# Optimization experiments

Measured on AMD Instinct MI355X. Metric: run time of the kernel, lower is better.

Reference implementation:

```python
import jax, jax.numpy as jnp
import numpy as np

H = 1024
NH = 16
HD = H // NH
TEMP = 0.5
LN_EPS = 1e-5


def setup_inputs() -> dict:
    key = jax.random.key(0)
    ks = jax.random.split(key, 11)
    s = 1.0 / np.sqrt(H)
    return {
        "feat": jax.random.normal(ks[0], (4, 2048, H), dtype=jnp.float32),
        "qw": jax.random.uniform(ks[1], (H, H), jnp.float32, -s, s),
        "qb": jax.random.uniform(ks[2], (H,), jnp.float32, -s, s),
        "kw": jax.random.uniform(ks[3], (H, H), jnp.float32, -s, s),
        "kb": jax.random.uniform(ks[4], (H,), jnp.float32, -s, s),
        "vw": jax.random.uniform(ks[5], (H, H), jnp.float32, -s, s),
        "vb": jax.random.uniform(ks[6], (H,), jnp.float32, -s, s),
        "ow": jax.random.uniform(ks[7], (H, H), jnp.float32, -s, s),
        "ob": jax.random.uniform(ks[8], (H,), jnp.float32, -s, s),
        "ln_g": jnp.ones((H,), jnp.float32),
        "ln_b": jnp.zeros((H,), jnp.float32),
    }


def reference(feat, qw, qb, kw, kb, vw, vb, ow, ob, ln_g, ln_b):
    B, S, _ = feat.shape
    # torch Linear: y = x @ W.T + b
    def split_heads(x):  # [B,S,H] -> [B,NH,S,HD]
        return x.reshape(B, S, NH, HD).transpose(0, 2, 1, 3)

    Q = split_heads(feat @ qw.T + qb)
    K = split_heads(feat @ kw.T + kb)
    V = split_heads(feat @ vw.T + vb)

    # temperature-scaled attention (note: divide by 0.5, NOT 1/sqrt(d))
    scores = jnp.einsum("bhqd,bhkd->bhqk", Q, K) / TEMP
    w = jax.nn.softmax(scores, axis=-1)
    attn = jnp.einsum("bhqk,bhkd->bhqd", w, V)  # [B,NH,S,HD]
    attn = attn.transpose(0, 2, 1, 3).reshape(B, S, H)

    out = attn @ ow.T + ob
    out = jax.nn.relu(out)  # dropout is identity in eval mode
    mu = jnp.mean(out, axis=-1, keepdims=True)
    var = jnp.mean(jnp.square(out - mu), axis=-1, keepdims=True)
    out = (out - mu) * jax.lax.rsqrt(var + LN_EPS) * ln_g + ln_b
    return out
```

## Files before the change

kernel.cpp:

```cpp
#include <hip/hip_runtime.h>
#include <math.h>

#define HDIM 1024
#define NHEAD 16
#define HEADD 64
#define SEQLEN 2048
#define BATCH 4
#define MROWS (BATCH * SEQLEN)
#define LN_EPS 1e-5f
#define QSCALE 2.8853900817779268f

typedef float f32x4 __attribute__((ext_vector_type(4)));
typedef short s16x8 __attribute__((ext_vector_type(8)));
typedef short s16x4 __attribute__((ext_vector_type(4)));
typedef __bf16 bf16x4 __attribute__((ext_vector_type(4)));

#define MFMA16(a, b, c) __builtin_amdgcn_mfma_f32_16x16x32_bf16((a), (b), (c), 0, 0, 0)

#if __has_builtin(__builtin_amdgcn_exp2f)
#define EXP2(x) __builtin_amdgcn_exp2f(x)
#else
#define EXP2(x) exp2f(x)
#endif

__device__ __forceinline__ void load_lds16(const __bf16* g, __bf16* l) {
  __builtin_amdgcn_global_load_lds((const __attribute__((address_space(1))) void*)g,
                                   (__attribute__((address_space(3))) void*)l, 16, 0, 0);
}

__global__ __launch_bounds__(256) void split_k(const float* __restrict__ src,
                                               __bf16* __restrict__ h,
                                               __bf16* __restrict__ l, int n4) {
  int i = blockIdx.x * blockDim.x + threadIdx.x;
  if (i >= n4) return;
  float4 v = reinterpret_cast<const float4*>(src)[i];
  bf16x4 hv, lv;
  hv[0] = (__bf16)v.x; hv[1] = (__bf16)v.y; hv[2] = (__bf16)v.z; hv[3] = (__bf16)v.w;
  lv[0] = (__bf16)(v.x - (float)hv[0]);
  lv[1] = (__bf16)(v.y - (float)hv[1]);
  lv[2] = (__bf16)(v.z - (float)hv[2]);
  lv[3] = (__bf16)(v.w - (float)hv[3]);
  reinterpret_cast<bf16x4*>(h)[i] = hv;
  reinterpret_cast<bf16x4*>(l)[i] = lv;
}

__global__ __launch_bounds__(256) void wsplit_k(
    const float* __restrict__ w0, const float* __restrict__ w1,
    const float* __restrict__ w2, const float* __restrict__ w3,
    __bf16* __restrict__ h0, __bf16* __restrict__ l0, __bf16* __restrict__ h1,
    __bf16* __restrict__ l1, __bf16* __restrict__ h2, __bf16* __restrict__ l2,
    __bf16* __restrict__ h3, __bf16* __restrict__ l3) {
  const int which = blockIdx.y;
  const float* src = which == 0 ? w0 : which == 1 ? w1 : which == 2 ? w2 : w3;
  __bf16* h = which == 0 ? h0 : which == 1 ? h1 : which == 2 ? h2 : h3;
  __bf16* l = which == 0 ? l0 : which == 1 ? l1 : which == 2 ? l2 : l3;
  const int i = blockIdx.x * blockDim.x + threadIdx.x;
  float4 v = reinterpret_cast<const float4*>(src)[i];
  bf16x4 hv, lv;
  hv[0] = (__bf16)v.x; hv[1] = (__bf16)v.y; hv[2] = (__bf16)v.z; hv[3] = (__bf16)v.w;
  lv[0] = (__bf16)(v.x - (float)hv[0]);
  lv[1] = (__bf16)(v.y - (float)hv[1]);
  lv[2] = (__bf16)(v.z - (float)hv[2]);
  lv[3] = (__bf16)(v.w - (float)hv[3]);
  reinterpret_cast<bf16x4*>(h)[i] = hv;
  reinterpret_cast<bf16x4*>(l)[i] = lv;
}

template <int EPI, int PASSES>
__global__ __launch_bounds__(256, PASSES == 2 ? 3 : 2) void gemm3p_k(
    const __bf16* __restrict__ AH, const __bf16* __restrict__ AL,
    const __bf16* __restrict__ BH, const __bf16* __restrict__ BL,
    const float* __restrict__ bias, const float scale, __bf16* __restrict__ CH,
    __bf16* __restrict__ CL, float* __restrict__ CF) {
  __shared__ __bf16 smem[(PASSES == 3) ? 32768 : 24576];

  const int tid = threadIdx.x;
  const int lane = tid & 63;
  const int w = tid >> 6;
  const int fr = lane & 15;
  const int g = lane >> 4;
  const int wm = w >> 1, wn = w & 1;
  const int m0 = blockIdx.x << 7;
  const int n0 = blockIdx.y << 7;

#define GSTAGE(buf, kt)                                                       \
  do {                                                                        \
    const int ke_ = (kt) * 32 + (lane & 3) * 8;                               \
    _Pragma("unroll") for (int c_ = 0; c_ < 2; ++c_) {                        \
      const int rr_ = 32 * w + 16 * c_ + (lane >> 2);                         \
      const int lo_ = (32 * w + 16 * c_) * 32;                                \
      load_lds16(AH + (size_t)(m0 + rr_) * HDIM + ke_, &smem[(buf)*4096 + lo_]); \
      load_lds16(AL + (size_t)(m0 + rr_) * HDIM + ke_, &smem[8192 + (buf)*4096 + lo_]); \
      load_lds16(BH + (size_t)(n0 + rr_) * HDIM + ke_, &smem[16384 + (buf)*4096 + lo_]); \
      if (PASSES == 3)                                                        \
        load_lds16(BL + (size_t)(n0 + rr_) * HDIM + ke_, &smem[24576 + (buf)*4096 + lo_]); \
    }                                                                         \
  } while (0)

  f32x4 acc[4][4] = {};

  GSTAGE(0, 0);
  __syncthreads();

  for (int kt = 0; kt < HDIM / 32; ++kt) {
    const int buf = kt & 1;
    if (kt + 1 < HDIM / 32) GSTAGE(buf ^ 1, kt + 1);

    s16x8 aH[4], aL[4], bH[4], bL[4];
#pragma unroll
    for (int mi = 0; mi < 4; ++mi) {
      const int off = (wm * 64 + mi * 16 + fr) * 32 + g * 8;
      aH[mi] = *reinterpret_cast<const s16x8*>(&smem[buf * 4096 + off]);
      aL[mi] = *reinterpret_cast<const s16x8*>(&smem[8192 + buf * 4096 + off]);
    }
#pragma unroll
    for (int ni = 0; ni < 4; ++ni) {
      const int off = (wn * 64 + ni * 16 + fr) * 32 + g * 8;
      bH[ni] = *reinterpret_cast<const s16x8*>(&smem[16384 + buf * 4096 + off]);
      if (PASSES == 3)
        bL[ni] = *reinterpret_cast<const s16x8*>(&smem[24576 + buf * 4096 + off]);
    }
#pragma unroll
    for (int mi = 0; mi < 4; ++mi)
#pragma unroll
      for (int ni = 0; ni < 4; ++ni) {
        acc[mi][ni] = MFMA16(aH[mi], bH[ni], acc[mi][ni]);
        if (PASSES == 3) acc[mi][ni] = MFMA16(aH[mi], bL[ni], acc[mi][ni]);
        acc[mi][ni] = MFMA16(aL[mi], bH[ni], acc[mi][ni]);
      }
    __syncthreads();
  }

  float bv[4];
#pragma unroll
  for (int ni = 0; ni < 4; ++ni) bv[ni] = bias[n0 + wn * 64 + ni * 16 + fr];

  if (EPI == 0) {
#pragma unroll
    for (int mi = 0; mi < 4; ++mi)
#pragma unroll
      for (int ni = 0; ni < 4; ++ni)
#pragma unroll
        for (int r = 0; r < 4; ++r) {
          const float v = (acc[mi][ni][r] + bv[ni]) * scale;
          const int m = m0 + wm * 64 + mi * 16 + 4 * g + r;
          const int n = n0 + wn * 64 + ni * 16 + fr;
          const int b = m >> 11, s = m & 2047, h = n >> 6, d = n & 63;
          const size_t o = ((size_t)(b * NHEAD + h) * SEQLEN + s) * HEADD + d;
          const __bf16 hb = (__bf16)v;
          CH[o] = hb;
          CL[o] = (__bf16)(v - (float)hb);
        }
  } else if (EPI == 2) {
#pragma unroll
    for (int mi = 0; mi < 4; ++mi)
#pragma unroll
      for (int ni = 0; ni < 4; ++ni)
#pragma unroll
        for (int r = 0; r < 4; ++r) {
          const int m = m0 + wm * 64 + mi * 16 + 4 * g + r;
          const int n = n0 + wn * 64 + ni * 16 + fr;
          CF[(size_t)m * HDIM + n] = acc[mi][ni][r] + bv[ni];
        }
  } else {
    __syncthreads();
#pragma unroll
    for (int mi = 0; mi < 4; ++mi)
#pragma unroll
      for (int ni = 0; ni < 4; ++ni)
#pragma unroll
        for (int r = 0; r < 4; ++r) {
          const float v = acc[mi][ni][r] + bv[ni];
          const int nl = wn * 64 + ni * 16 + fr;
          const int ml = wm * 64 + mi * 16 + 4 * g + r;
          smem[nl * 128 + (((ml >> 3) ^ (nl & 7)) << 3) + (ml & 7)] = (__bf16)v;
        }
    __syncthreads();
    const int nl = tid >> 1, mh = tid & 1;
    const int b = m0 >> 11, s0 = m0 & 2047;
    const int gn = n0 + nl, h = gn >> 6, d = gn & 63;
#pragma unroll
    for (int j = 0; j < 8; ++j) {
      const int cm = mh * 8 + j;
      s16x8 vv = *reinterpret_cast<const s16x8*>(&smem[nl * 128 + ((cm ^ (nl & 7)) << 3)]);
      const size_t o = ((size_t)((b * NHEAD + h) * HEADD + d)) * SEQLEN + s0 + cm * 8;
      *reinterpret_cast<s16x8*>(&CH[o]) = vv;
    }
  }
#undef GSTAGE
}

__global__ __launch_bounds__(256, 2) void attn6_k(
    const __bf16* __restrict__ QH, const __bf16* __restrict__ QL,
    const __bf16* __restrict__ KH, const __bf16* __restrict__ KL,
    const __bf16* __restrict__ VT, __bf16* __restrict__ OH,
    __bf16* __restrict__ OL) {
  __shared__ __bf16 smem[32768];

  const int tid = threadIdx.x;
  const int lane = tid & 63;
  const int w = tid >> 6;
  const int fr = lane & 15;
  const int g = lane >> 4;
  const int f7 = fr & 7;

  const int blk = blockIdx.x;
  const int xcd = blk & 7, idx = blk >> 3;
  const int bh = xcd * 8 + (idx >> 4);
  const int qt = idx & 15;
  const int q0 = qt << 7;
  const size_t bhO = (size_t)bh * SEQLEN * HEADD;

  s16x8 qHf[2][2], qLf[2][2];
#pragma unroll
  for (int qb = 0; qb < 2; ++qb) {
    const size_t qoff = bhO + (size_t)(q0 + w * 32 + qb * 16 + fr) * HEADD;
#pragma unroll
    for (int ks = 0; ks < 2; ++ks) {
      qHf[qb][ks] = *reinterpret_cast<const s16x8*>(&QH[qoff + ks * 32 + g * 8]);
      qLf[qb][ks] = *reinterpret_cast<const s16x8*>(&QL[qoff + ks * 32 + g * 8]);
    }
  }

  const __bf16* gsrc[6];
  int gstep[6], ldoff[6];
  {
    const int rsub = lane >> 3;
    const int ch = (lane & 7) ^ rsub;
#pragma unroll
    for (int i_ = 0; i_ < 6; ++i_) {
      const int L_ = w * 6 + i_;
      const int t_ = L_ >> 3, sub_ = L_ & 7;
      ldoff[i_] = t_ * 8192 + sub_ * 512;
      if (t_ < 2) {
        const __bf16* base_ = (t_ == 0) ? KH : KL;
        gsrc[i_] = base_ + bhO + (size_t)(sub_ * 8 + rsub) * HEADD + ch * 8;
        gstep[i_] = 64 * HEADD;
      } else {
        gsrc[i_] = VT + ((size_t)bh * HEADD + sub_ * 8 + rsub) * SEQLEN + ch * 8;
        gstep[i_] = 64;
      }
    }
  }

#define ASTAGE(bufl)                                              \
  do {                                                            \
    _Pragma("unroll") for (int i_ = 0; i_ < 6; ++i_) {            \
      load_lds16(gsrc[i_], &smem[ldoff[i_] + (bufl)*4096]);       \
      gsrc[i_] += gstep[i_];                                      \
    }                                                             \
  } while (0)

  const int rb0 = fr * 64 + ((g ^ f7) << 3);
  const int rb1 = fr * 64 + (((4 + g) ^ f7) << 3);
  const int prbase = 24576 + w * 2048;
  const int pwbase = 24576 + w * 2048 + fr * 64 + (g & 1) * 4;
  int pco[4];
#pragma unroll
  for (int kb = 0; kb < 4; ++kb) pco[kb] = ((2 * kb + (g >> 1)) ^ f7) << 3;

  f32x4 oacc0[4] = {}, oacc1[4] = {};
  float m0r = -1e30f, m1r = -1e30f, l0r = 0.f, l1r = 0.f;

  auto process = [&](const int B) {
    f32x4 sf0[4] = {}, sf1[4] = {};
    __builtin_amdgcn_s_setprio(1);
#pragma unroll
    for (int kb = 0; kb < 4; ++kb) {
      const s16x8 kh0 = *reinterpret_cast<const s16x8*>(&smem[B * 4096 + kb * 1024 + rb0]);
      const s16x8 kl0 = *reinterpret_cast<const s16x8*>(&smem[8192 + B * 4096 + kb * 1024 + rb0]);
      const s16x8 kh1 = *reinterpret_cast<const s16x8*>(&smem[B * 4096 + kb * 1024 + rb1]);
      const s16x8 kl1 = *reinterpret_cast<const s16x8*>(&smem[8192 + B * 4096 + kb * 1024 + rb1]);
      sf0[kb] = MFMA16(kh0, qHf[0][0], sf0[kb]);
      sf0[kb] = MFMA16(kl0, qHf[0][0], sf0[kb]);
      sf0[kb] = MFMA16(kh0, qLf[0][0], sf0[kb]);
      sf0[kb] = MFMA16(kh1, qHf[0][1], sf0[kb]);
      sf0[kb] = MFMA16(kl1, qHf[0][1], sf0[kb]);
      sf0[kb] = MFMA16(kh1, qLf[0][1], sf0[kb]);
      sf1[kb] = MFMA16(kh0, qHf[1][0], sf1[kb]);
      sf1[kb] = MFMA16(kl0, qHf[1][0], sf1[kb]);
      sf1[kb] = MFMA16(kh0, qLf[1][0], sf1[kb]);
      sf1[kb] = MFMA16(kh1, qHf[1][1], sf1[kb]);
      sf1[kb] = MFMA16(kl1, qHf[1][1], sf1[kb]);
      sf1[kb] = MFMA16(kh1, qLf[1][1], sf1[kb]);
    }
    __builtin_amdgcn_s_setprio(0);

    float mx0 = sf0[0][0], mx1 = sf1[0][0];
#pragma unroll
    for (int kb = 0; kb < 4; ++kb)
#pragma unroll
      for (int r = 0; r < 4; ++r) {
        mx0 = fmaxf(mx0, sf0[kb][r]);
        mx1 = fmaxf(mx1, sf1[kb][r]);
      }
    mx0 = fmaxf(mx0, __shfl_xor(mx0, 16));
    mx0 = fmaxf(mx0, __shfl_xor(mx0, 32));
    mx1 = fmaxf(mx1, __shfl_xor(mx1, 16));
    mx1 = fmaxf(mx1, __shfl_xor(mx1, 32));
    const bool ok = (mx0 <= m0r + 11.5f) && (mx1 <= m1r + 11.5f);
    if (!__all(ok)) {
      const float mn0 = fmaxf(m0r, mx0), mn1 = fmaxf(m1r, mx1);
      const float c0 = EXP2(m0r - mn0), c1 = EXP2(m1r - mn1);
      m0r = mn0; m1r = mn1;
      l0r *= c0; l1r *= c1;
      float cr0[4], cr1[4];
#pragma unroll
      for (int r = 0; r < 4; ++r) {
        cr0[r] = __shfl(c0, 4 * g + r);
        cr1[r] = __shfl(c1, 4 * g + r);
      }
#pragma unroll
      for (int di = 0; di < 4; ++di)
#pragma unroll
        for (int r = 0; r < 4; ++r) {
          oacc0[di][r] *= cr0[r];
          oacc1[di][r] *= cr1[r];
        }
    }
    float ps0 = 0.f, ps1 = 0.f;
#pragma unroll
    for (int kb = 0; kb < 4; ++kb)
#pragma unroll
      for (int r = 0; r < 4; ++r) {
        const float p0 = EXP2(sf0[kb][r] - m0r);
        const float p1 = EXP2(sf1[kb][r] - m1r);
        sf0[kb][r] = p0;
        sf1[kb][r] = p1;
        ps0 += p0;
        ps1 += p1;
      }
    ps0 += __shfl_xor(ps0, 16);
    ps0 += __shfl_xor(ps0, 32);
    ps1 += __shfl_xor(ps1, 16);
    ps1 += __shfl_xor(ps1, 32);
    l0r += ps0;
    l1r += ps1;

#pragma unroll
    for (int kb = 0; kb < 4; ++kb) {
      s16x4 h0, h1;
#pragma unroll
      for (int r = 0; r < 4; ++r) {
        h0[r] = __builtin_bit_cast(short, (__bf16)sf0[kb][r]);
        h1[r] = __builtin_bit_cast(short, (__bf16)sf1[kb][r]);
      }
      *reinterpret_cast<s16x4*>(&smem[pwbase + pco[kb]]) = h0;
      *reinterpret_cast<s16x4*>(&smem[pwbase + 1024 + pco[kb]]) = h1;
    }

    __builtin_amdgcn_s_setprio(1);
#pragma unroll
    for (int ks = 0; ks < 2; ++ks) {
      const int rbv = ks ? rb1 : rb0;
      const s16x8 p0 = *reinterpret_cast<const s16x8*>(&smem[prbase + rbv]);
      const s16x8 p1 = *reinterpret_cast<const s16x8*>(&smem[prbase + 1024 + rbv]);
#pragma unroll
      for (int di = 0; di < 4; ++di) {
        const s16x8 vf = *reinterpret_cast<const s16x8*>(
            &smem[16384 + B * 4096 + di * 1024 + rbv]);
        oacc0[di] = MFMA16(p0, vf, oacc0[di]);
        oacc1[di] = MFMA16(p1, vf, oacc1[di]);
      }
    }
    __builtin_amdgcn_s_setprio(0);
  };

  ASTAGE(0);
  __syncthreads();
  for (int kt = 0; kt < SEQLEN / 64 - 2; kt += 2) {
    ASTAGE(1);
    process(0);
    __syncthreads();
    ASTAGE(0);
    process(1);
    __syncthreads();
  }
  ASTAGE(1);
  process(0);
  __syncthreads();
  process(1);

  const int b = bh >> 4, h = bh & 15;
  const float inv0 = 1.0f / l0r, inv1 = 1.0f / l1r;
  float iv0[4], iv1[4];
#pragma unroll
  for (int r = 0; r < 4; ++r) {
    iv0[r] = __shfl(inv0, 4 * g + r);
    iv1[r] = __shfl(inv1, 4 * g + r);
  }
#pragma unroll
  for (int di = 0; di < 4; ++di)
#pragma unroll
    for (int r = 0; r < 4; ++r) {
      const int srow = q0 + w * 32 + 4 * g + r;
      const size_t o0 = ((size_t)b * SEQLEN + srow) * HDIM + h * 64 + di * 16 + fr;
      const size_t o1 = o0 + 16 * HDIM;
      const float v0 = oacc0[di][r] * iv0[r];
      const float v1 = oacc1[di][r] * iv1[r];
      const __bf16 hb0 = (__bf16)v0;
      const __bf16 hb1 = (__bf16)v1;
      OH[o0] = hb0;
      OL[o0] = (__bf16)(v0 - (float)hb0);
      OH[o1] = hb1;
      OL[o1] = (__bf16)(v1 - (float)hb1);
    }
#undef ASTAGE
}

__global__ __launch_bounds__(256) void relu_ln_k(const float* __restrict__ X,
                                                 const float* __restrict__ gam,
                                                 const float* __restrict__ bta,
                                                 float* __restrict__ out) {
  __shared__ float red[8];
  const int row = blockIdx.x;
  const int tid = threadIdx.x;
  const int c = tid << 2;

  const float4 v = *reinterpret_cast<const float4*>(&X[(size_t)row * HDIM + c]);
  float x[4] = {fmaxf(v.x, 0.f), fmaxf(v.y, 0.f), fmaxf(v.z, 0.f), fmaxf(v.w, 0.f)};
  float sum = x[0] + x[1] + x[2] + x[3];
  float ss = x[0] * x[0] + x[1] * x[1] + x[2] * x[2] + x[3] * x[3];
#pragma unroll
  for (int off = 1; off < 64; off <<= 1) {
    sum += __shfl_xor(sum, off);
    ss += __shfl_xor(ss, off);
  }
  const int wid = tid >> 6;
  if ((tid & 63) == 0) {
    red[wid] = sum;
    red[4 + wid] = ss;
  }
  __syncthreads();
  sum = red[0] + red[1] + red[2] + red[3];
  ss = red[4] + red[5] + red[6] + red[7];
  const float mean = sum * (1.0f / HDIM);
  const float var = ss * (1.0f / HDIM) - mean * mean;
  const float rstd = rsqrtf(var + LN_EPS);

  const float4 gv = *reinterpret_cast<const float4*>(&gam[c]);
  const float4 bv = *reinterpret_cast<const float4*>(&bta[c]);
  float4 o;
  o.x = (x[0] - mean) * rstd * gv.x + bv.x;
  o.y = (x[1] - mean) * rstd * gv.y + bv.y;
  o.z = (x[2] - mean) * rstd * gv.z + bv.z;
  o.w = (x[3] - mean) * rstd * gv.w + bv.w;
  *reinterpret_cast<float4*>(&out[(size_t)row * HDIM + c]) = o;
}

extern "C" void kernel_launch(void* const* d_in, const int* in_sizes, int n_in,
                              void* d_out, int out_size, void* d_ws, size_t ws_size,
                              hipStream_t stream) {
  const float* feat = (const float*)d_in[0];
  const float* qw = (const float*)d_in[1];
  const float* qb = (const float*)d_in[2];
  const float* kw = (const float*)d_in[3];
  const float* kb = (const float*)d_in[4];
  const float* vw = (const float*)d_in[5];
  const float* vb = (const float*)d_in[6];
  const float* ow = (const float*)d_in[7];
  const float* ob = (const float*)d_in[8];
  const float* ln_g = (const float*)d_in[9];
  const float* ln_b = (const float*)d_in[10];

  char* ws = (char*)d_ws;
  const size_t MB = 1u << 20;
  __bf16* qwH = (__bf16*)(ws + 0 * MB);
  __bf16* kwH = (__bf16*)(ws + 2 * MB);
  __bf16* vwH = (__bf16*)(ws + 4 * MB);
  __bf16* owH = (__bf16*)(ws + 6 * MB);
  __bf16* qwL = (__bf16*)(ws + 8 * MB);
  __bf16* kwL = (__bf16*)(ws + 10 * MB);
  __bf16* vwL = (__bf16*)(ws + 12 * MB);
  __bf16* owL = (__bf16*)(ws + 14 * MB);
  __bf16* QHp = (__bf16*)(ws + 16 * MB);
  __bf16* QLp = (__bf16*)(ws + 32 * MB);
  __bf16* KHp = (__bf16*)(ws + 48 * MB);
  __bf16* KLp = (__bf16*)(ws + 64 * MB);
  __bf16* VTp = (__bf16*)(ws + 80 * MB);
  __bf16* ftH = (__bf16*)(ws + 96 * MB);
  __bf16* ftL = (__bf16*)(ws + 112 * MB);
  __bf16* atH = ftH;
  __bf16* atL = ftL;
  float* proj = (float*)(ws + 16 * MB);

  split_k<<<(MROWS * HDIM / 4 + 255) / 256, 256, 0, stream>>>(feat, ftH, ftL,
                                                              MROWS * HDIM / 4);
  wsplit_k<<<dim3(HDIM * HDIM / 4 / 256, 4), 256, 0, stream>>>(
      qw, kw, vw, ow, qwH, qwL, kwH, kwL, vwH, vwL, owH, owL);

  const dim3 gg(MROWS / 128, HDIM / 128);
  gemm3p_k<0, 3><<<gg, 256, 0, stream>>>(ftH, ftL, qwH, qwL, qb, QSCALE, QHp, QLp, nullptr);
  gemm3p_k<0, 3><<<gg, 256, 0, stream>>>(ftH, ftL, kwH, kwL, kb, 1.0f, KHp, KLp, nullptr);
  gemm3p_k<1, 2><<<gg, 256, 0, stream>>>(ftH, ftL, vwH, vwL, vb, 1.0f, VTp, nullptr, nullptr);

  attn6_k<<<BATCH * NHEAD * (SEQLEN / 128), 256, 0, stream>>>(QHp, QLp, KHp, KLp,
                                                              VTp, atH, atL);

  gemm3p_k<2, 2><<<gg, 256, 0, stream>>>(atH, atL, owH, owL, ob, 1.0f, nullptr,
                                         nullptr, proj);

  relu_ln_k<<<MROWS, 256, 0, stream>>>(proj, ln_g, ln_b, (float*)d_out);
}
```

Before: 451.5 us.

## Keep softmax probabilities in registers by permuting K rows, dropping P LDS staging

The attention kernel now reorders which K rows each lane reads, using a new swizzle on the K load and read offsets. This makes the score MFMA output layout match the A-operand layout the PV MFMA expects, so the probabilities are packed straight from registers into bf16 operands. That removes the per-tile P write to and read from shared memory and cuts LDS use from 64KB to 48KB, with launch bounds raised to 3 blocks per CU. The GEMM launch bound for the 2-pass variant is also lowered from 3 to 2, which may change its register allocation and occupancy.

```diff
diff --git a/kernel.cpp b/kernel.cpp
--- a/kernel.cpp
+++ b/kernel.cpp
@@ -67,7 +67,7 @@
 }
 
 template <int EPI, int PASSES>
-__global__ __launch_bounds__(256, PASSES == 2 ? 3 : 2) void gemm3p_k(
+__global__ __launch_bounds__(256, 2) void gemm3p_k(
     const __bf16* __restrict__ AH, const __bf16* __restrict__ AL,
     const __bf16* __restrict__ BH, const __bf16* __restrict__ BL,
     const float* __restrict__ bias, const float scale, __bf16* __restrict__ CH,
@@ -190,12 +190,12 @@
 #undef GSTAGE
 }
 
-__global__ __launch_bounds__(256, 2) void attn6_k(
+__global__ __launch_bounds__(256, 3) void attn7_k(
     const __bf16* __restrict__ QH, const __bf16* __restrict__ QL,
     const __bf16* __restrict__ KH, const __bf16* __restrict__ KL,
     const __bf16* __restrict__ VT, __bf16* __restrict__ OH,
     __bf16* __restrict__ OL) {
-  __shared__ __bf16 smem[32768];
+  __shared__ __bf16 smem[24576];
 
   const int tid = threadIdx.x;
   const int lane = tid & 63;
@@ -226,7 +226,7 @@
   int gstep[6], ldoff[6];
   {
     const int rsub = lane >> 3;
-    const int ch = (lane & 7) ^ rsub;
+    const int l7 = lane & 7;
 #pragma unroll
     for (int i_ = 0; i_ < 6; ++i_) {
       const int L_ = w * 6 + i_;
@@ -234,10 +234,12 @@
       ldoff[i_] = t_ * 8192 + sub_ * 512;
       if (t_ < 2) {
         const __bf16* base_ = (t_ == 0) ? KH : KL;
-        gsrc[i_] = base_ + bhO + (size_t)(sub_ * 8 + rsub) * HEADD + ch * 8;
+        const int ch_ = l7 ^ (((sub_ & 3) << 1) | (rsub & 1));
+        gsrc[i_] = base_ + bhO + (size_t)(sub_ * 8 + rsub) * HEADD + ch_ * 8;
         gstep[i_] = 64 * HEADD;
       } else {
-        gsrc[i_] = VT + ((size_t)bh * HEADD + sub_ * 8 + rsub) * SEQLEN + ch * 8;
+        const int ch_ = l7 ^ rsub;
+        gsrc[i_] = VT + ((size_t)bh * HEADD + sub_ * 8 + rsub) * SEQLEN + ch_ * 8;
         gstep[i_] = 64;
       }
     }
@@ -251,13 +253,11 @@
     }                                                             \
   } while (0)
 
-  const int rb0 = fr * 64 + ((g ^ f7) << 3);
-  const int rb1 = fr * 64 + (((4 + g) ^ f7) << 3);
-  const int prbase = 24576 + w * 2048;
-  const int pwbase = 24576 + w * 2048 + fr * 64 + (g & 1) * 4;
-  int pco[4];
-#pragma unroll
-  for (int kb = 0; kb < 4; ++kb) pco[kb] = ((2 * kb + (g >> 1)) ^ f7) << 3;
+  const int sK = ((fr >> 2) << 1) | (fr & 1);
+  const int rbk0 = ((fr >> 2) * 8 + (fr & 3)) * 64 + ((g ^ sK) << 3);
+  const int rbk1 = rbk0 ^ 32;
+  const int rbv0 = fr * 64 + ((g ^ f7) << 3);
+  const int rbv1 = rbv0 ^ 32;
 
   f32x4 oacc0[4] = {}, oacc1[4] = {};
   float m0r = -1e30f, m1r = -1e30f, l0r = 0.f, l1r = 0.f;
@@ -267,10 +267,11 @@
     __builtin_amdgcn_s_setprio(1);
 #pragma unroll
     for (int kb = 0; kb < 4; ++kb) {
-      const s16x8 kh0 = *reinterpret_cast<const s16x8*>(&smem[B * 4096 + kb * 1024 + rb0]);
-      const s16x8 kl0 = *reinterpret_cast<const s16x8*>(&smem[8192 + B * 4096 + kb * 1024 + rb0]);
-      const s16x8 kh1 = *reinterpret_cast<const s16x8*>(&smem[B * 4096 + kb * 1024 + rb1]);
-      const s16x8 kl1 = *reinterpret_cast<const s16x8*>(&smem[8192 + B * 4096 + kb * 1024 + rb1]);
+      const int ko = (kb & 1) * 256 + (kb >> 1) * 2048;
+      const s16x8 kh0 = *reinterpret_cast<const s16x8*>(&smem[B * 4096 + ko + rbk0]);
+      const s16x8 kl0 = *reinterpret_cast<const s16x8*>(&smem[8192 + B * 4096 + ko + rbk0]);
+      const s16x8 kh1 = *reinterpret_cast<const s16x8*>(&smem[B * 4096 + ko + rbk1]);
+      const s16x8 kl1 = *reinterpret_cast<const s16x8*>(&smem[8192 + B * 4096 + ko + rbk1]);
       sf0[kb] = MFMA16(kh0, qHf[0][0], sf0[kb]);
       sf0[kb] = MFMA16(kl0, qHf[0][0], sf0[kb]);
       sf0[kb] = MFMA16(kh0, qLf[0][0], sf0[kb]);
@@ -337,30 +338,24 @@
     l0r += ps0;
     l1r += ps1;
 
-#pragma unroll
-    for (int kb = 0; kb < 4; ++kb) {
-      s16x4 h0, h1;
-#pragma unroll
-      for (int r = 0; r < 4; ++r) {
-        h0[r] = __builtin_bit_cast(short, (__bf16)sf0[kb][r]);
-        h1[r] = __builtin_bit_cast(short, (__bf16)sf1[kb][r]);
-      }
-      *reinterpret_cast<s16x4*>(&smem[pwbase + pco[kb]]) = h0;
-      *reinterpret_cast<s16x4*>(&smem[pwbase + 1024 + pco[kb]]) = h1;
-    }
-
     __builtin_amdgcn_s_setprio(1);
 #pragma unroll
     for (int ks = 0; ks < 2; ++ks) {
-      const int rbv = ks ? rb1 : rb0;
-      const s16x8 p0 = *reinterpret_cast<const s16x8*>(&smem[prbase + rbv]);
-      const s16x8 p1 = *reinterpret_cast<const s16x8*>(&smem[prbase + 1024 + rbv]);
+      s16x8 pa0, pa1;
+#pragma unroll
+      for (int i = 0; i < 4; ++i) {
+        pa0[i]     = __builtin_bit_cast(short, (__bf16)sf0[2 * ks][i]);
+        pa0[i + 4] = __builtin_bit_cast(short, (__bf16)sf0[2 * ks + 1][i]);
+        pa1[i]     = __builtin_bit_cast(short, (__bf16)sf1[2 * ks][i]);
+        pa1[i + 4] = __builtin_bit_cast(short, (__bf16)sf1[2 * ks + 1][i]);
+      }
+      const int rbv = ks ? rbv1 : rbv0;
 #pragma unroll
       for (int di = 0; di < 4; ++di) {
         const s16x8 vf = *reinterpret_cast<const s16x8*>(
             &smem[16384 + B * 4096 + di * 1024 + rbv]);
-        oacc0[di] = MFMA16(p0, vf, oacc0[di]);
-        oacc1[di] = MFMA16(p1, vf, oacc1[di]);
+        oacc0[di] = MFMA16(pa0, vf, oacc0[di]);
+        oacc1[di] = MFMA16(pa1, vf, oacc1[di]);
       }
     }
     __builtin_amdgcn_s_setprio(0);
@@ -494,7 +489,7 @@
   gemm3p_k<0, 3><<<gg, 256, 0, stream>>>(ftH, ftL, kwH, kwL, kb, 1.0f, KHp, KLp, nullptr);
   gemm3p_k<1, 2><<<gg, 256, 0, stream>>>(ftH, ftL, vwH, vwL, vb, 1.0f, VTp, nullptr, nullptr);
 
-  attn6_k<<<BATCH * NHEAD * (SEQLEN / 128), 256, 0, stream>>>(QHp, QLp, KHp, KLp,
+  attn7_k<<<BATCH * NHEAD * (SEQLEN / 128), 256, 0, stream>>>(QHp, QLp, KHp, KLp,
                                                               VTp, atH, atL);
 
   gemm3p_k<2, 2><<<gg, 256, 0, stream>>>(atH, atL, owH, owL, ob, 1.0f, nullptr,
```

After: 443.9 us. About the same (-1.7%).
